# Optimization experiments

Hardware: AMD Instinct MI355X
Metric: run time of the kernel (lower is better)

The kernel has to match this reference:

```python
import jax, jax.numpy as jnp
import numpy as np

B = 8        # graphs per batch
N = 6000     # nodes per graph
DEG = 8      # avg degree -> E = B*N*DEG edges
K1, K2, K3 = 3600, 2160, 1080   # ceil(0.6*6000), ceil(0.6*3600), ceil(0.5*2160)
EPS = 1e-5
C_IN = 512


def gcn_conv(x, row, col, w, W, b):
    # GCNConv, normalize=True, add_self_loops=False. deg computed on col (target).
    n = x.shape[0]
    deg = jnp.zeros((n,), x.dtype).at[col].add(w)
    dinv = jnp.where(deg > 0, jax.lax.rsqrt(jnp.maximum(deg, 1e-12)), 0.0)
    norm = dinv[row] * w * dinv[col]                      # [E]
    h = x @ W                                             # [n, out]
    out = jnp.zeros_like(h).at[col].add(norm[:, None] * h[row])
    return out + b


def batch_norm(x, g, b):
    # track_running_stats=False -> always batch stats, biased variance
    mu = jnp.mean(x, 0)
    var = jnp.mean((x - mu) ** 2, 0)
    return (x - mu) * jax.lax.rsqrt(var + EPS) * g + b


def sag_pool(x, row, col, w, Wrel, Wroot, bias, n_per_graph, k):
    # SAGPooling: score = GraphConv(x, edge)->1, perm = per-graph top-k,
    # x = x[perm] * tanh(score[perm]); edges filtered (masked via weight 0 here).
    n = x.shape[0]
    agg = jnp.zeros_like(x).at[col].add(w[:, None] * x[row])
    score = (agg @ Wrel + x @ Wroot).squeeze(-1) + bias[0]        # [n]
    s2 = score.reshape(B, n_per_graph)
    _, topi = jax.lax.top_k(s2, k)                                # [B, k]
    perm = (topi + jnp.arange(B)[:, None] * n_per_graph).reshape(-1)
    x_new = x[perm] * jnp.tanh(score[perm])[:, None]
    inv = jnp.full((n,), -1, jnp.int32).at[perm].set(jnp.arange(B * k, dtype=jnp.int32))
    nrow = inv[row]
    ncol = inv[col]
    valid = (nrow >= 0) & (ncol >= 0) & (w > 0)
    w_new = jnp.where(valid, w, 0.0)
    nrow = jnp.where(valid, nrow, 0)
    ncol = jnp.where(valid, ncol, 0)
    return x_new, nrow, ncol, w_new


def setup_inputs() -> dict:
    key = jax.random.key(0)
    ks = jax.random.split(key, 32)
    x = jax.random.normal(ks[0], (B * N, C_IN), jnp.float32)
    src = jax.random.randint(ks[1], (B, N * DEG), 0, N)
    dst = jax.random.randint(ks[2], (B, N * DEG), 0, N)
    off = jnp.arange(B)[:, None] * N
    edge_index = jnp.stack([(src + off).reshape(-1), (dst + off).reshape(-1)]).astype(jnp.int32)

    def lin(k, cin, cout):
        return jax.random.normal(k, (cin, cout), jnp.float32) * (1.0 / np.sqrt(cin))

    inp = {
        'x': x, 'edge_index': edge_index,
        'W1': lin(ks[3], 512, 512), 'b1': jnp.zeros((512,), jnp.float32),
        'g1': jnp.ones((512,), jnp.float32), 'be1': jnp.zeros((512,), jnp.float32),
        'p1_rel': lin(ks[4], 512, 1), 'p1_root': lin(ks[5], 512, 1), 'p1_b': jnp.zeros((1,), jnp.float32),
        'W2': lin(ks[6], 512, 512), 'b2': jnp.zeros((512,), jnp.float32),
        'g2': jnp.ones((512,), jnp.float32), 'be2': jnp.zeros((512,), jnp.float32),
        'p2_rel': lin(ks[7], 512, 1), 'p2_root': lin(ks[8], 512, 1), 'p2_b': jnp.zeros((1,), jnp.float32),
        'W3': lin(ks[9], 512, 256), 'b3': jnp.zeros((256,), jnp.float32),
        'g3': jnp.ones((256,), jnp.float32), 'be3': jnp.zeros((256,), jnp.float32),
        'p3_rel': lin(ks[10], 256, 1), 'p3_root': lin(ks[11], 256, 1), 'p3_b': jnp.zeros((1,), jnp.float32),
        'W4': lin(ks[12], 256, 256), 'b4': jnp.zeros((256,), jnp.float32),
        'fcW': lin(ks[13], 512, 1), 'fcb': jnp.zeros((1,), jnp.float32),
    }
    return inp


def reference(x, edge_index, W1, b1, g1, be1, p1_rel, p1_root, p1_b,
              W2, b2, g2, be2, p2_rel, p2_root, p2_b,
              W3, b3, g3, be3, p3_rel, p3_root, p3_b,
              W4, b4, fcW, fcb):
    row, col = edge_index[0], edge_index[1]
    w = jnp.ones((row.shape[0],), jnp.float32)

    h = jax.nn.relu(batch_norm(gcn_conv(x, row, col, w, W1, b1), g1, be1))
    h, row, col, w = sag_pool(h, row, col, w, p1_rel, p1_root, p1_b, N, K1)

    h = jax.nn.relu(batch_norm(gcn_conv(h, row, col, w, W2, b2), g2, be2))
    h, row, col, w = sag_pool(h, row, col, w, p2_rel, p2_root, p2_b, K1, K2)

    h = jax.nn.relu(batch_norm(gcn_conv(h, row, col, w, W3, b3), g3, be3))
    h, row, col, w = sag_pool(h, row, col, w, p3_rel, p3_root, p3_b, K2, K3)

    h = gcn_conv(h, row, col, w, W4, b4)        # [B*K3, 256]
    g = h.reshape(B, K3, 256)
    feature = jnp.concatenate([g.max(axis=1), g.mean(axis=1)], axis=1)  # [B, 512]
    out = feature @ fcW + fcb
    return out, feature
```

## Files before the change

kernel.cpp:

```cpp
#include <hip/hip_runtime.h>
#include <cstdint>
#include <cstddef>

#define NB 8
#define NPG0 6000
#define N0 48000
#define NE 384000
#define KP1 3600
#define KP2 2160
#define KP3 1080

typedef __attribute__((ext_vector_type(8))) short short8;
typedef __attribute__((ext_vector_type(4))) float f32x4;
typedef __attribute__((ext_vector_type(4))) unsigned int u32x4;

__device__ inline ushort f2bf(float v) {
  unsigned u = __float_as_uint(v);
  u += 0x7FFF + ((u >> 16) & 1);
  return (ushort)(u >> 16);
}
__device__ inline float bf2f(ushort h) { return __uint_as_float(((unsigned)h) << 16); }

__global__ void split_kernel(const float* __restrict__ x, ushort* __restrict__ hi,
                             ushort* __restrict__ lo, size_t n4) {
  size_t i = (size_t)blockIdx.x * blockDim.x + threadIdx.x;
  size_t stride = (size_t)gridDim.x * blockDim.x;
  for (; i < n4; i += stride) {
    float4 v = ((const float4*)x)[i];
    ushort4 h, l;
    h.x = f2bf(v.x); l.x = f2bf(v.x - bf2f(h.x));
    h.y = f2bf(v.y); l.y = f2bf(v.y - bf2f(h.y));
    h.z = f2bf(v.z); l.z = f2bf(v.z - bf2f(h.z));
    h.w = f2bf(v.w); l.w = f2bf(v.w - bf2f(h.w));
    ((ushort4*)hi)[i] = h;
    ((ushort4*)lo)[i] = l;
  }
}

__global__ void wsplit_kernel(const float* __restrict__ W, ushort* __restrict__ hiT,
                              ushort* __restrict__ loT, int K, int N) {
  __shared__ float tile[32][33];
  int k0 = blockIdx.y * 32, n0 = blockIdx.x * 32;
  int tx = threadIdx.x;
  for (int dy = threadIdx.y; dy < 32; dy += 8)
    tile[dy][tx] = W[(size_t)(k0 + dy) * N + n0 + tx];
  __syncthreads();
  for (int dy = threadIdx.y; dy < 32; dy += 8) {
    float v = tile[tx][dy];
    ushort h = f2bf(v);
    ushort l = f2bf(v - bf2f(h));
    hiT[(size_t)(n0 + dy) * K + k0 + tx] = h;
    loT[(size_t)(n0 + dy) * K + k0 + tx] = l;
  }
}

__global__ __launch_bounds__(256) void gemm_split(
    const ushort* __restrict__ Ahi, const ushort* __restrict__ Alo,
    const ushort* __restrict__ BThi, const ushort* __restrict__ BTlo,
    float* __restrict__ C, int M, int K, int N, int mblocks) {
  __shared__ u32x4 lds4[2048];
  const int tid = threadIdx.x;
  const int mblk = blockIdx.x % mblocks;
  const int nblk = blockIdx.x / mblocks;
  const int bm = mblk * 128, bn = nblk * 128;
  const int lane = tid & 63;
  const int w = tid >> 6;
  const int wr = w >> 1, wc = w & 1;

  const ushort* sptr[8];
  int ldschunk[8];
#pragma unroll
  for (int i = 0; i < 8; ++i) {
    int idx = i * 256 + tid;
    int g = idx >> 9;
    int p = idx & 511;
    int r = p >> 2, pc = p & 3;
    int grow;
    const ushort* base;
    if (g == 0)      { base = Ahi;  grow = min(bm + r, M - 1); }
    else if (g == 1) { base = Alo;  grow = min(bm + r, M - 1); }
    else if (g == 2) { base = BThi; grow = bn + r; }
    else             { base = BTlo; grow = bn + r; }
    sptr[i] = base + (size_t)grow * K + pc * 8;
    int swz = (r & 3) ^ ((r >> 2) & 3);
    ldschunk[i] = g * 512 + r * 4 + (pc ^ swz);
  }

  f32x4 acc[4][4];
#pragma unroll
  for (int m = 0; m < 4; ++m)
#pragma unroll
    for (int n = 0; n < 4; ++n) acc[m][n] = (f32x4){0.f, 0.f, 0.f, 0.f};

  u32x4 st[8];
#pragma unroll
  for (int i = 0; i < 8; ++i) st[i] = *(const u32x4*)(sptr[i]);

  const int nk = K >> 5;
  for (int t = 0; t < nk; ++t) {
    __syncthreads();
#pragma unroll
    for (int i = 0; i < 8; ++i) lds4[ldschunk[i]] = st[i];
    if (t + 1 < nk) {
#pragma unroll
      for (int i = 0; i < 8; ++i) st[i] = *(const u32x4*)(sptr[i] + (size_t)(t + 1) * 32);
    }
    __syncthreads();

    const int kb = lane >> 4;
    const int l15 = lane & 15;
    short8 bh[4], bl[4];
#pragma unroll
    for (int n = 0; n < 4; ++n) {
      int rB = wc * 64 + n * 16 + l15;
      int swz = (rB & 3) ^ ((rB >> 2) & 3);
      int ch = rB * 4 + (kb ^ swz);
      bh[n] = *(const short8*)&lds4[1024 + ch];
      bl[n] = *(const short8*)&lds4[1536 + ch];
    }
#pragma unroll
    for (int m = 0; m < 4; ++m) {
      int rA = wr * 64 + m * 16 + l15;
      int swz = (rA & 3) ^ ((rA >> 2) & 3);
      int ch = rA * 4 + (kb ^ swz);
      short8 ah = *(const short8*)&lds4[ch];
      short8 al = *(const short8*)&lds4[512 + ch];
#pragma unroll
      for (int n = 0; n < 4; ++n) {
        acc[m][n] = __builtin_amdgcn_mfma_f32_16x16x32_bf16(ah, bh[n], acc[m][n], 0, 0, 0);
        acc[m][n] = __builtin_amdgcn_mfma_f32_16x16x32_bf16(ah, bl[n], acc[m][n], 0, 0, 0);
        acc[m][n] = __builtin_amdgcn_mfma_f32_16x16x32_bf16(al, bh[n], acc[m][n], 0, 0, 0);
      }
    }
  }

#pragma unroll
  for (int m = 0; m < 4; ++m) {
    int gr0 = bm + wr * 64 + m * 16 + ((lane >> 4) << 2);
#pragma unroll
    for (int j = 0; j < 4; ++j) {
      int gr = gr0 + j;
      if (gr < M) {
#pragma unroll
        for (int n = 0; n < 4; ++n) {
          C[(size_t)gr * N + bn + wc * 64 + n * 16 + (lane & 15)] = acc[m][n][j];
        }
      }
    }
  }
}

__global__ void edge_count_kernel(const int* __restrict__ col, const float* __restrict__ w,
                                  int E, int* __restrict__ counts) {
  int i = blockIdx.x * blockDim.x + threadIdx.x;
  if (i >= E) return;
  if (w && !(w[i] > 0.f)) return;
  atomicAdd(&counts[col[i]], 1);
}

__global__ __launch_bounds__(1024) void scan_kernel(const int* __restrict__ counts,
                                                    int* __restrict__ offsets, int n) {
  __shared__ int wsum[16];
  int tid = threadIdx.x;
  int per = (n + 1023) / 1024;
  int beg = tid * per;
  int end = min(beg + per, n);
  int s = 0;
  for (int i = beg; i < end; ++i) s += counts[i];
  int lane = tid & 63, wid = tid >> 6;
  int v = s;
  for (int off = 1; off < 64; off <<= 1) {
    int t = __shfl_up(v, off);
    if (lane >= off) v += t;
  }
  if (lane == 63) wsum[wid] = v;
  __syncthreads();
  if (wid == 0) {
    int wv = (lane < 16) ? wsum[lane] : 0;
    for (int off = 1; off < 16; off <<= 1) {
      int t = __shfl_up(wv, off);
      if (lane >= off) wv += t;
    }
    if (lane < 16) wsum[lane] = wv;
  }
  __syncthreads();
  int base = (v - s) + (wid > 0 ? wsum[wid - 1] : 0);
  int run = base;
  for (int i = beg; i < end; ++i) {
    offsets[i] = run;
    run += counts[i];
  }
  if (tid == 1023) offsets[n] = run;
}

__global__ void csr_fill_kernel(const int* __restrict__ row, const int* __restrict__ col,
                                const float* __restrict__ w, int E,
                                const int* __restrict__ offsets, int* __restrict__ fill,
                                int* __restrict__ csr_src) {
  int i = blockIdx.x * blockDim.x + threadIdx.x;
  if (i >= E) return;
  if (w && !(w[i] > 0.f)) return;
  int c = col[i];
  int pos = offsets[c] + atomicAdd(&fill[c], 1);
  csr_src[pos] = row[i];
}

__global__ void dinv_kernel(const int* __restrict__ counts, float* __restrict__ dinv, int n) {
  int i = blockIdx.x * blockDim.x + threadIdx.x;
  if (i >= n) return;
  int c = counts[i];
  dinv[i] = (c > 0) ? (1.0f / sqrtf((float)c)) : 0.f;
}

__global__ __launch_bounds__(256) void gcn_gather_kernel(
    const float* __restrict__ G, const int* __restrict__ offsets,
    const int* __restrict__ csr_src, const float* __restrict__ dinv,
    const float* __restrict__ bias, float* __restrict__ out, int C, int n) {
  int wid = threadIdx.x >> 6, lane = threadIdx.x & 63;
  int t = blockIdx.x * 4 + wid;
  if (t >= n) return;
  int beg = offsets[t], end = offsets[t + 1];
  float dt = dinv[t];
  bool two = (C == 512);
  float4 acc0 = make_float4(0.f, 0.f, 0.f, 0.f);
  float4 acc1 = make_float4(0.f, 0.f, 0.f, 0.f);
  for (int e = beg; e < end; ++e) {
    int s = csr_src[e];
    float ds = dinv[s];
    const float4* hr = (const float4*)(G + (size_t)s * C);
    float4 v0 = hr[lane];
    acc0.x += ds * v0.x; acc0.y += ds * v0.y; acc0.z += ds * v0.z; acc0.w += ds * v0.w;
    if (two) {
      float4 v1 = hr[lane + 64];
      acc1.x += ds * v1.x; acc1.y += ds * v1.y; acc1.z += ds * v1.z; acc1.w += ds * v1.w;
    }
  }
  float4* op = (float4*)(out + (size_t)t * C);
  float4 b0 = bias ? ((const float4*)bias)[lane] : make_float4(0.f, 0.f, 0.f, 0.f);
  op[lane] = make_float4(dt * acc0.x + b0.x, dt * acc0.y + b0.y,
                         dt * acc0.z + b0.z, dt * acc0.w + b0.w);
  if (two) {
    op[lane + 64] = make_float4(dt * acc1.x, dt * acc1.y, dt * acc1.z, dt * acc1.w);
  }
}

__global__ __launch_bounds__(256) void bn_stats_kernel(
    const float* __restrict__ h, size_t n4, int C, float* __restrict__ sums) {
  __shared__ float ls[1024];
  for (int i = threadIdx.x; i < 2 * C; i += 256) ls[i] = 0.f;
  __syncthreads();
  const int c0 = (threadIdx.x * 4) & (C - 1);
  float s0 = 0.f, s1 = 0.f, s2 = 0.f, s3 = 0.f;
  float q0 = 0.f, q1 = 0.f, q2 = 0.f, q3 = 0.f;
  size_t i = (size_t)blockIdx.x * 256 + threadIdx.x;
  const size_t stride = (size_t)gridDim.x * 256;
  for (; i < n4; i += stride) {
    float4 v = ((const float4*)h)[i];
    s0 += v.x; q0 += v.x * v.x;
    s1 += v.y; q1 += v.y * v.y;
    s2 += v.z; q2 += v.z * v.z;
    s3 += v.w; q3 += v.w * v.w;
  }
  atomicAdd(&ls[c0 + 0], s0); atomicAdd(&ls[C + c0 + 0], q0);
  atomicAdd(&ls[c0 + 1], s1); atomicAdd(&ls[C + c0 + 1], q1);
  atomicAdd(&ls[c0 + 2], s2); atomicAdd(&ls[C + c0 + 2], q2);
  atomicAdd(&ls[c0 + 3], s3); atomicAdd(&ls[C + c0 + 3], q3);
  __syncthreads();
  for (int j = threadIdx.x; j < 2 * C; j += 256) atomicAdd(&sums[j], ls[j]);
}

__global__ void bn_finalize_kernel(const float* __restrict__ sums,
                                   const float* __restrict__ g,
                                   const float* __restrict__ be,
                                   int n, int C, float* __restrict__ ss) {
  int c = blockIdx.x * blockDim.x + threadIdx.x;
  if (c >= C) return;
  float inv_n = 1.0f / (float)n;
  float mean = sums[c] * inv_n;
  float var = sums[C + c] * inv_n - mean * mean;
  var = fmaxf(var, 0.f);
  float sc = g[c] * rsqrtf(var + 1e-5f);
  ss[c] = sc;
  ss[C + c] = be[c] - mean * sc;
}

__global__ __launch_bounds__(256) void bn_dots_kernel(
    float* __restrict__ h, const float* __restrict__ ss,
    const float* __restrict__ wrel, const float* __restrict__ wroot,
    float* __restrict__ u, float* __restrict__ rr, int n, int C) {
  int wid = threadIdx.x >> 6, lane = threadIdx.x & 63;
  int v = blockIdx.x * 4 + wid;
  if (v >= n) return;
  float4* hr = (float4*)(h + (size_t)v * C);
  int nf4 = C >> 2;
  float su = 0.f, sr = 0.f;
  for (int q = lane; q < nf4; q += 64) {
    float4 x = hr[q];
    int c = q << 2;
    float4 sc = *(const float4*)&ss[c];
    float4 sh = *(const float4*)&ss[C + c];
    x.x = fmaxf(fmaf(x.x, sc.x, sh.x), 0.f);
    x.y = fmaxf(fmaf(x.y, sc.y, sh.y), 0.f);
    x.z = fmaxf(fmaf(x.z, sc.z, sh.z), 0.f);
    x.w = fmaxf(fmaf(x.w, sc.w, sh.w), 0.f);
    hr[q] = x;
    float4 w1 = *(const float4*)&wrel[c];
    float4 w2 = *(const float4*)&wroot[c];
    su += x.x * w1.x + x.y * w1.y + x.z * w1.z + x.w * w1.w;
    sr += x.x * w2.x + x.y * w2.y + x.z * w2.z + x.w * w2.w;
  }
  for (int off = 32; off > 0; off >>= 1) {
    su += __shfl_down(su, off);
    sr += __shfl_down(sr, off);
  }
  if (lane == 0) {
    u[v] = su;
    rr[v] = sr;
  }
}

__global__ void score_kernel(const float* __restrict__ u, const float* __restrict__ rr,
                             const int* __restrict__ offsets, const int* __restrict__ csr_src,
                             const float* __restrict__ pb, float* __restrict__ score, int n) {
  int i = blockIdx.x * blockDim.x + threadIdx.x;
  if (i >= n) return;
  float s = rr[i] + pb[0];
  int beg = offsets[i], end = offsets[i + 1];
  for (int e = beg; e < end; ++e) s += u[csr_src[e]];
  score[i] = s;
}

__global__ __launch_bounds__(1024) void topk_radix_kernel(
    const float* __restrict__ score, int npg, int K, int* __restrict__ perm) {
  __shared__ unsigned sbuf[8192];
  __shared__ int tieL[6000];
  __shared__ int hist[256];
  __shared__ int wps[4];
  __shared__ unsigned sPref;
  __shared__ int sKrem, sAbove, sSel, sTie;
  int g = blockIdx.x;
  int tid = threadIdx.x;
  for (int i = tid; i < npg; i += 1024) {
    unsigned u = __float_as_uint(score[g * npg + i]);
    sbuf[i] = (u >> 31) ? ~u : (u | 0x80000000u);
  }
  if (tid == 0) { sPref = 0; sKrem = K; sAbove = 0; sSel = 0; sTie = 0; }
  __syncthreads();

  for (int pass = 0; pass < 4; ++pass) {
    int shift = 24 - 8 * pass;
    if (tid < 256) hist[tid] = 0;
    unsigned prefLoc = sPref;
    int kRemLoc = sKrem;
    __syncthreads();
    for (int i = tid; i < npg; i += 1024) {
      unsigned k = sbuf[i];
      if (pass == 0 || (k >> (shift + 8)) == prefLoc)
        atomicAdd(&hist[(k >> shift) & 255], 1);
    }
    __syncthreads();
    int v = 0, a = 0;
    if (tid < 256) {
      a = hist[255 - tid];
      v = a;
      int lane = tid & 63;
      for (int off = 1; off < 64; off <<= 1) {
        int t2 = __shfl_up(v, off);
        if (lane >= off) v += t2;
      }
      if (lane == 63) wps[tid >> 6] = v;
    }
    __syncthreads();
    if (tid < 256) {
      int w4 = tid >> 6;
      int incl = v;
      for (int q = 0; q < w4; ++q) incl += wps[q];
      int gt = incl - a;
      if (gt < kRemLoc && kRemLoc <= incl) {
        int d = 255 - tid;
        sPref = (prefLoc << 8) | (unsigned)d;
        sAbove += gt;
        sKrem = kRemLoc - gt;
      }
    }
    __syncthreads();
  }

  unsigned T = sPref;
  int above = sAbove;
  for (int i = tid; i < npg; i += 1024) {
    unsigned k = sbuf[i];
    if (k > T) {
      int p = atomicAdd(&sSel, 1);
      perm[g * K + p] = g * npg + i;
    } else if (k == T) {
      int p = atomicAdd(&sTie, 1);
      tieL[p] = i;
    }
  }
  __syncthreads();
  int r = sKrem, tc = sTie;
  if (r == tc) {
    for (int j = tid; j < r; j += 1024) perm[g * K + above + j] = g * npg + tieL[j];
  } else {
    int p2 = 1;
    while (p2 < tc) p2 <<= 1;
    for (int i = tid; i < p2; i += 1024) sbuf[i] = (i < tc) ? (unsigned)tieL[i] : 0xFFFFFFFFu;
    __syncthreads();
    for (int k2 = 2; k2 <= p2; k2 <<= 1) {
      for (int j = k2 >> 1; j > 0; j >>= 1) {
        for (int i = tid; i < p2; i += 1024) {
          int l = i ^ j;
          if (l > i) {
            unsigned a2 = sbuf[i], b2 = sbuf[l];
            bool up = ((i & k2) == 0);
            if (up ? (a2 > b2) : (a2 < b2)) { sbuf[i] = b2; sbuf[l] = a2; }
          }
        }
        __syncthreads();
      }
    }
    for (int j = tid; j < r; j += 1024) perm[g * K + above + j] = g * npg + (int)sbuf[j];
  }
}

__global__ void inv_set_kernel(const int* __restrict__ perm, int* __restrict__ inv, int m) {
  int i = blockIdx.x * blockDim.x + threadIdx.x;
  if (i < m) inv[perm[i]] = i;
}

__global__ void xnew_split_kernel(const float* __restrict__ h, const float* __restrict__ score,
                                  const int* __restrict__ perm, ushort* __restrict__ xhi,
                                  ushort* __restrict__ xlo, int C) {
  int i = blockIdx.x;
  int old = perm[i];
  float tv = tanhf(score[old]);
  const float4* src = (const float4*)(h + (size_t)old * C);
  int c4 = C >> 2;
  for (int c = threadIdx.x; c < c4; c += blockDim.x) {
    float4 v = src[c];
    v.x *= tv; v.y *= tv; v.z *= tv; v.w *= tv;
    ushort4 hh, ll;
    hh.x = f2bf(v.x); ll.x = f2bf(v.x - bf2f(hh.x));
    hh.y = f2bf(v.y); ll.y = f2bf(v.y - bf2f(hh.y));
    hh.z = f2bf(v.z); ll.z = f2bf(v.z - bf2f(hh.z));
    hh.w = f2bf(v.w); ll.w = f2bf(v.w - bf2f(hh.w));
    ((ushort4*)(xhi + (size_t)i * C))[c] = hh;
    ((ushort4*)(xlo + (size_t)i * C))[c] = ll;
  }
}

__global__ void edge_remap_count_kernel(const int* __restrict__ row, const int* __restrict__ col,
                                        const float* __restrict__ w, const int* __restrict__ inv,
                                        int E, int* __restrict__ nrow, int* __restrict__ ncol,
                                        float* __restrict__ nw, int* __restrict__ counts) {
  int i = blockIdx.x * blockDim.x + threadIdx.x;
  if (i >= E) return;
  float wv = w ? w[i] : 1.f;
  int nr = inv[row[i]];
  int nc = inv[col[i]];
  bool valid = (nr >= 0) && (nc >= 0) && (wv > 0.f);
  nrow[i] = valid ? nr : 0;
  ncol[i] = valid ? nc : 0;
  nw[i] = valid ? wv : 0.f;
  if (valid) atomicAdd(&counts[nc], 1);
}

__global__ void final_pool_kernel(const float* __restrict__ h, float* __restrict__ dout) {
  int g = blockIdx.x;
  int c = threadIdx.x;
  const float* base = h + ((size_t)g * KP3) * 256 + c;
  float mx = -3.402823466e38f, sm = 0.f;
  for (int r = 0; r < KP3; ++r) {
    float v = base[(size_t)r * 256];
    mx = fmaxf(mx, v);
    sm += v;
  }
  dout[8 + g * 512 + c] = mx;
  dout[8 + g * 512 + 256 + c] = sm * (1.0f / (float)KP3);
}

__global__ void fc_kernel(const float* __restrict__ feat, const float* __restrict__ fcW,
                          const float* __restrict__ fcb, float* __restrict__ dout) {
  int g = blockIdx.x;
  int lane = threadIdx.x;
  float s = 0.f;
  for (int c = lane; c < 512; c += 64) s += feat[g * 512 + c] * fcW[c];
  for (int off = 32; off > 0; off >>= 1) s += __shfl_down(s, off);
  if (lane == 0) dout[g] = s + fcb[0];
}

static inline size_t alignup(size_t x) { return (x + 255) & ~(size_t)255; }

extern "C" void kernel_launch(void* const* d_in, const int* in_sizes, int n_in,
                              void* d_out, int out_size, void* d_ws, size_t ws_size,
                              hipStream_t stream) {
  (void)in_sizes; (void)n_in; (void)out_size; (void)ws_size;
  const float* x0 = (const float*)d_in[0];
  const int* ei = (const int*)d_in[1];
  const int* row0 = ei;
  const int* col0 = ei + NE;
  const float* W1 = (const float*)d_in[2];
  const float* g1 = (const float*)d_in[4];
  const float* be1 = (const float*)d_in[5];
  const float* p1rel = (const float*)d_in[6];
  const float* p1root = (const float*)d_in[7];
  const float* p1b = (const float*)d_in[8];
  const float* W2 = (const float*)d_in[9];
  const float* g2 = (const float*)d_in[11];
  const float* be2 = (const float*)d_in[12];
  const float* p2rel = (const float*)d_in[13];
  const float* p2root = (const float*)d_in[14];
  const float* p2b = (const float*)d_in[15];
  const float* W3 = (const float*)d_in[16];
  const float* g3 = (const float*)d_in[18];
  const float* be3 = (const float*)d_in[19];
  const float* p3rel = (const float*)d_in[20];
  const float* p3root = (const float*)d_in[21];
  const float* p3b = (const float*)d_in[22];
  const float* W4 = (const float*)d_in[23];
  const float* b4 = (const float*)d_in[24];
  const float* fcW = (const float*)d_in[25];
  const float* fcb = (const float*)d_in[26];
  float* out = (float*)d_out;

  char* ws = (char*)d_ws;
  size_t off = 0;
  auto alloc = [&](size_t bytes) {
    char* p = ws + off;
    off = alignup(off + bytes);
    return p;
  };
  float* RegA = (float*)alloc((size_t)N0 * 512 * 4);
  float* RegB = (float*)alloc((size_t)N0 * 512 * 4);
  ushort* Ahi = (ushort*)alloc((size_t)N0 * 512 * 2);
  ushort* Alo = (ushort*)alloc((size_t)N0 * 512 * 2);
  int* rowA = (int*)alloc((size_t)NE * 4);
  int* colA = (int*)alloc((size_t)NE * 4);
  float* wA = (float*)alloc((size_t)NE * 4);
  int* rowB = (int*)alloc((size_t)NE * 4);
  int* colB = (int*)alloc((size_t)NE * 4);
  float* wB = (float*)alloc((size_t)NE * 4);
  int* csr_src = (int*)alloc((size_t)NE * 4);
  int* offsets = (int*)alloc((size_t)(N0 + 1) * 4);
  int* counts = (int*)alloc((size_t)N0 * 4);
  int* fill = (int*)alloc((size_t)N0 * 4);
  float* dinv = (float*)alloc((size_t)N0 * 4);
  float* scoreb = (float*)alloc((size_t)N0 * 4);
  float* ubuf = (float*)alloc((size_t)N0 * 4);
  float* rbuf = (float*)alloc((size_t)N0 * 4);
  int* perm = (int*)alloc((size_t)NB * KP1 * 4);
  int* inv = (int*)alloc((size_t)N0 * 4);
  float* bnsums = (float*)alloc(1024 * 4);
  float* bnss = (float*)alloc(1024 * 4);
  ushort* wt1h = (ushort*)alloc(512 * 512 * 2);
  ushort* wt1l = (ushort*)alloc(512 * 512 * 2);
  ushort* wt2h = (ushort*)alloc(512 * 512 * 2);
  ushort* wt2l = (ushort*)alloc(512 * 512 * 2);
  ushort* wt3h = (ushort*)alloc(256 * 512 * 2);
  ushort* wt3l = (ushort*)alloc(256 * 512 * 2);
  ushort* wt4h = (ushort*)alloc(256 * 256 * 2);
  ushort* wt4l = (ushort*)alloc(256 * 256 * 2);

  const int n1 = NB * KP1;
  const int n2 = NB * KP2;
  const int n3 = NB * KP3;

  auto build_csr_rest = [&](const int* row, const int* col, const float* w, int n) {
    hipMemsetAsync(fill, 0, (size_t)n * 4, stream);
    scan_kernel<<<1, 1024, 0, stream>>>(counts, offsets, n);
    csr_fill_kernel<<<(NE + 255) / 256, 256, 0, stream>>>(row, col, w, NE, offsets, fill, csr_src);
    dinv_kernel<<<(n + 255) / 256, 256, 0, stream>>>(counts, dinv, n);
  };

  auto bn_relu_dots = [&](float* h, int n, int C, const float* g, const float* be,
                          const float* wrel, const float* wroot) {
    hipMemsetAsync(bnsums, 0, 4096, stream);
    size_t n4 = (size_t)n * C / 4;
    int nblk = (int)min((n4 + 255) / 256, (size_t)512);
    bn_stats_kernel<<<nblk, 256, 0, stream>>>(h, n4, C, bnsums);
    bn_finalize_kernel<<<(C + 255) / 256, 256, 0, stream>>>(bnsums, g, be, n, C, bnss);
    bn_dots_kernel<<<(n + 3) / 4, 256, 0, stream>>>(h, bnss, wrel, wroot, ubuf, rbuf, n, C);
  };

  auto gemm = [&](const ushort* ah, const ushort* al, const ushort* bth, const ushort* btl,
                  float* Cout, int M, int K, int N) {
    int mblocks = (M + 127) / 128;
    int nblocks = N / 128;
    gemm_split<<<mblocks * nblocks, 256, 0, stream>>>(ah, al, bth, btl, Cout, M, K, N, mblocks);
  };

  auto pool = [&](const float* h, int n, int C, int npg, int K, const float* pb, int nNext,
                  const int* erow, const int* ecol, const float* ew,
                  int* nrow, int* ncol, float* nw) {
    score_kernel<<<(n + 255) / 256, 256, 0, stream>>>(ubuf, rbuf, offsets, csr_src, pb, scoreb, n);
    topk_radix_kernel<<<NB, 1024, 0, stream>>>(scoreb, npg, K, perm);
    hipMemsetAsync(inv, 0xFF, (size_t)n * 4, stream);
    hipMemsetAsync(counts, 0, (size_t)nNext * 4, stream);
    inv_set_kernel<<<(NB * K + 255) / 256, 256, 0, stream>>>(perm, inv, NB * K);
    xnew_split_kernel<<<NB * K, 128, 0, stream>>>(h, scoreb, perm, Ahi, Alo, C);
    edge_remap_count_kernel<<<(NE + 255) / 256, 256, 0, stream>>>(erow, ecol, ew, inv, NE,
                                                                  nrow, ncol, nw, counts);
  };

  wsplit_kernel<<<dim3(512 / 32, 512 / 32), dim3(32, 8), 0, stream>>>(W1, wt1h, wt1l, 512, 512);
  wsplit_kernel<<<dim3(512 / 32, 512 / 32), dim3(32, 8), 0, stream>>>(W2, wt2h, wt2l, 512, 512);
  wsplit_kernel<<<dim3(256 / 32, 512 / 32), dim3(32, 8), 0, stream>>>(W3, wt3h, wt3l, 512, 256);
  wsplit_kernel<<<dim3(256 / 32, 256 / 32), dim3(32, 8), 0, stream>>>(W4, wt4h, wt4l, 256, 256);
  split_kernel<<<4096, 256, 0, stream>>>(x0, Ahi, Alo, (size_t)N0 * 512 / 4);

  hipMemsetAsync(counts, 0, (size_t)N0 * 4, stream);
  edge_count_kernel<<<(NE + 255) / 256, 256, 0, stream>>>(col0, nullptr, NE, counts);
  build_csr_rest(row0, col0, nullptr, N0);
  gemm(Ahi, Alo, wt1h, wt1l, RegA, N0, 512, 512);
  gcn_gather_kernel<<<(N0 + 3) / 4, 256, 0, stream>>>(RegA, offsets, csr_src, dinv, nullptr,
                                                      RegB, 512, N0);
  bn_relu_dots(RegB, N0, 512, g1, be1, p1rel, p1root);
  pool(RegB, N0, 512, NPG0, KP1, p1b, n1, row0, col0, nullptr, rowA, colA, wA);

  build_csr_rest(rowA, colA, wA, n1);
  gemm(Ahi, Alo, wt2h, wt2l, RegA, n1, 512, 512);
  gcn_gather_kernel<<<(n1 + 3) / 4, 256, 0, stream>>>(RegA, offsets, csr_src, dinv, nullptr,
                                                      RegB, 512, n1);
  bn_relu_dots(RegB, n1, 512, g2, be2, p2rel, p2root);
  pool(RegB, n1, 512, KP1, KP2, p2b, n2, rowA, colA, wA, rowB, colB, wB);

  build_csr_rest(rowB, colB, wB, n2);
  gemm(Ahi, Alo, wt3h, wt3l, RegA, n2, 512, 256);
  gcn_gather_kernel<<<(n2 + 3) / 4, 256, 0, stream>>>(RegA, offsets, csr_src, dinv, nullptr,
                                                      RegB, 256, n2);
  bn_relu_dots(RegB, n2, 256, g3, be3, p3rel, p3root);
  pool(RegB, n2, 256, KP2, KP3, p3b, n3, rowB, colB, wB, rowA, colA, wA);

  build_csr_rest(rowA, colA, wA, n3);
  gemm(Ahi, Alo, wt4h, wt4l, RegA, n3, 256, 256);
  gcn_gather_kernel<<<(n3 + 3) / 4, 256, 0, stream>>>(RegA, offsets, csr_src, dinv, b4,
                                                      RegB, 256, n3);

  final_pool_kernel<<<NB, 256, 0, stream>>>(RegB, out);
  fc_kernel<<<NB, 64, 0, stream>>>(out + 8, fcW, fcb, out);
}
```

Baseline: 1.064 ms.

## Use direct global-to-LDS double buffering in GEMM and fuse small graph kernels

The split-bf16 GEMM now loads tiles with global_load_lds straight into a double-buffered LDS region, prefetching the next K slice during compute and dropping one barrier per iteration. The dinv computation moves into the scan kernel and the inv scatter into xnew_split, which removes two launches per stage. The gather kernel interleaves blocks across graphs and unrolls its edge loop by two for more memory-level parallelism. The costs are doubled LDS per block, which may lower occupancy, and the gather grid now assumes node counts divisible by four.

```diff
diff --git a/kernel.cpp b/kernel.cpp
--- a/kernel.cpp
+++ b/kernel.cpp
@@ -20,6 +20,12 @@
   return (ushort)(u >> 16);
 }
 __device__ inline float bf2f(ushort h) { return __uint_as_float(((unsigned)h) << 16); }
+
+__device__ __forceinline__ void glds16(const void* g, void* l) {
+  __builtin_amdgcn_global_load_lds(
+      (const __attribute__((address_space(1))) unsigned int*)g,
+      (__attribute__((address_space(3))) unsigned int*)l, 16, 0, 0);
+}
 
 __global__ void split_kernel(const float* __restrict__ x, ushort* __restrict__ hi,
                              ushort* __restrict__ lo, size_t n4) {
@@ -58,32 +64,26 @@
     const ushort* __restrict__ Ahi, const ushort* __restrict__ Alo,
     const ushort* __restrict__ BThi, const ushort* __restrict__ BTlo,
     float* __restrict__ C, int M, int K, int N, int mblocks) {
-  __shared__ u32x4 lds4[2048];
+  __shared__ u32x4 lds4[4096];
   const int tid = threadIdx.x;
+  const int lane = tid & 63;
+  const int w = tid >> 6;
   const int mblk = blockIdx.x % mblocks;
   const int nblk = blockIdx.x / mblocks;
   const int bm = mblk * 128, bn = nblk * 128;
-  const int lane = tid & 63;
-  const int w = tid >> 6;
   const int wr = w >> 1, wc = w & 1;
 
-  const ushort* sptr[8];
-  int ldschunk[8];
-#pragma unroll
-  for (int i = 0; i < 8; ++i) {
-    int idx = i * 256 + tid;
-    int g = idx >> 9;
-    int p = idx & 511;
-    int r = p >> 2, pc = p & 3;
-    int grow;
-    const ushort* base;
-    if (g == 0)      { base = Ahi;  grow = min(bm + r, M - 1); }
-    else if (g == 1) { base = Alo;  grow = min(bm + r, M - 1); }
-    else if (g == 2) { base = BThi; grow = bn + r; }
-    else             { base = BTlo; grow = bn + r; }
-    sptr[i] = base + (size_t)grow * K + pc * 8;
-    int swz = (r & 3) ^ ((r >> 2) & 3);
-    ldschunk[i] = g * 512 + r * 4 + (pc ^ swz);
+  const ushort* srcp[8];
+  {
+    const ushort* base = (w == 0) ? Ahi : (w == 1) ? Alo : (w == 2) ? BThi : BTlo;
+    #pragma unroll
+    for (int i = 0; i < 8; ++i) {
+      int r = i * 16 + (lane >> 2);
+      int swz = (r & 3) ^ ((r >> 2) & 3);
+      int pcs = (lane & 3) ^ swz;
+      int grow = (w < 2) ? min(bm + r, M - 1) : (bn + r);
+      srcp[i] = base + (size_t)grow * K + pcs * 8;
+    }
   }
 
   f32x4 acc[4][4];
@@ -92,39 +92,39 @@
 #pragma unroll
     for (int n = 0; n < 4; ++n) acc[m][n] = (f32x4){0.f, 0.f, 0.f, 0.f};
 
-  u32x4 st[8];
-#pragma unroll
-  for (int i = 0; i < 8; ++i) st[i] = *(const u32x4*)(sptr[i]);
-
   const int nk = K >> 5;
+  const int kb = lane >> 4;
+  const int l15 = lane & 15;
+
+#pragma unroll
+  for (int i = 0; i < 8; ++i) glds16(srcp[i], &lds4[w * 512 + i * 64]);
+  __syncthreads();
+
+  int cur = 0;
   for (int t = 0; t < nk; ++t) {
-    __syncthreads();
-#pragma unroll
-    for (int i = 0; i < 8; ++i) lds4[ldschunk[i]] = st[i];
     if (t + 1 < nk) {
-#pragma unroll
-      for (int i = 0; i < 8; ++i) st[i] = *(const u32x4*)(sptr[i] + (size_t)(t + 1) * 32);
-    }
-    __syncthreads();
-
-    const int kb = lane >> 4;
-    const int l15 = lane & 15;
+      int nb = (cur ^ 1) * 2048;
+#pragma unroll
+      for (int i = 0; i < 8; ++i)
+        glds16(srcp[i] + (size_t)(t + 1) * 32, &lds4[nb + w * 512 + i * 64]);
+    }
+    const int bb = cur * 2048;
     short8 bh[4], bl[4];
 #pragma unroll
     for (int n = 0; n < 4; ++n) {
       int rB = wc * 64 + n * 16 + l15;
       int swz = (rB & 3) ^ ((rB >> 2) & 3);
       int ch = rB * 4 + (kb ^ swz);
-      bh[n] = *(const short8*)&lds4[1024 + ch];
-      bl[n] = *(const short8*)&lds4[1536 + ch];
+      bh[n] = *(const short8*)&lds4[bb + 1024 + ch];
+      bl[n] = *(const short8*)&lds4[bb + 1536 + ch];
     }
 #pragma unroll
     for (int m = 0; m < 4; ++m) {
       int rA = wr * 64 + m * 16 + l15;
       int swz = (rA & 3) ^ ((rA >> 2) & 3);
       int ch = rA * 4 + (kb ^ swz);
-      short8 ah = *(const short8*)&lds4[ch];
-      short8 al = *(const short8*)&lds4[512 + ch];
+      short8 ah = *(const short8*)&lds4[bb + ch];
+      short8 al = *(const short8*)&lds4[bb + 512 + ch];
 #pragma unroll
       for (int n = 0; n < 4; ++n) {
         acc[m][n] = __builtin_amdgcn_mfma_f32_16x16x32_bf16(ah, bh[n], acc[m][n], 0, 0, 0);
@@ -132,6 +132,8 @@
         acc[m][n] = __builtin_amdgcn_mfma_f32_16x16x32_bf16(al, bh[n], acc[m][n], 0, 0, 0);
       }
     }
+    __syncthreads();
+    cur ^= 1;
   }
 
 #pragma unroll
@@ -159,7 +161,8 @@
 }
 
 __global__ __launch_bounds__(1024) void scan_kernel(const int* __restrict__ counts,
-                                                    int* __restrict__ offsets, int n) {
+                                                    int* __restrict__ offsets,
+                                                    float* __restrict__ dinv, int n) {
   __shared__ int wsum[16];
   int tid = threadIdx.x;
   int per = (n + 1023) / 1024;
@@ -188,7 +191,9 @@
   int run = base;
   for (int i = beg; i < end; ++i) {
     offsets[i] = run;
-    run += counts[i];
+    int c = counts[i];
+    run += c;
+    dinv[i] = (c > 0) ? rsqrtf((float)c) : 0.f;
   }
   if (tid == 1023) offsets[n] = run;
 }
@@ -205,34 +210,46 @@
   csr_src[pos] = row[i];
 }
 
-__global__ void dinv_kernel(const int* __restrict__ counts, float* __restrict__ dinv, int n) {
-  int i = blockIdx.x * blockDim.x + threadIdx.x;
-  if (i >= n) return;
-  int c = counts[i];
-  dinv[i] = (c > 0) ? (1.0f / sqrtf((float)c)) : 0.f;
-}
-
 __global__ __launch_bounds__(256) void gcn_gather_kernel(
     const float* __restrict__ G, const int* __restrict__ offsets,
     const int* __restrict__ csr_src, const float* __restrict__ dinv,
-    const float* __restrict__ bias, float* __restrict__ out, int C, int n) {
+    const float* __restrict__ bias, float* __restrict__ out, int C, int n, int npg) {
   int wid = threadIdx.x >> 6, lane = threadIdx.x & 63;
-  int t = blockIdx.x * 4 + wid;
+  int g = blockIdx.x & 7;
+  int local = blockIdx.x >> 3;
+  int t = g * npg + local * 4 + wid;
   if (t >= n) return;
   int beg = offsets[t], end = offsets[t + 1];
   float dt = dinv[t];
   bool two = (C == 512);
   float4 acc0 = make_float4(0.f, 0.f, 0.f, 0.f);
   float4 acc1 = make_float4(0.f, 0.f, 0.f, 0.f);
-  for (int e = beg; e < end; ++e) {
-    int s = csr_src[e];
-    float ds = dinv[s];
-    const float4* hr = (const float4*)(G + (size_t)s * C);
-    float4 v0 = hr[lane];
-    acc0.x += ds * v0.x; acc0.y += ds * v0.y; acc0.z += ds * v0.z; acc0.w += ds * v0.w;
+  int e = beg;
+  for (; e + 2 <= end; e += 2) {
+    int s0 = csr_src[e], s1 = csr_src[e + 1];
+    float d0 = dinv[s0], d1 = dinv[s1];
+    const float4* h0 = (const float4*)(G + (size_t)s0 * C);
+    const float4* h1 = (const float4*)(G + (size_t)s1 * C);
+    float4 a0 = h0[lane];
+    float4 b0 = h1[lane];
+    acc0.x += d0 * a0.x; acc0.y += d0 * a0.y; acc0.z += d0 * a0.z; acc0.w += d0 * a0.w;
+    acc0.x += d1 * b0.x; acc0.y += d1 * b0.y; acc0.z += d1 * b0.z; acc0.w += d1 * b0.w;
     if (two) {
-      float4 v1 = hr[lane + 64];
-      acc1.x += ds * v1.x; acc1.y += ds * v1.y; acc1.z += ds * v1.z; acc1.w += ds * v1.w;
+      float4 a1 = h0[lane + 64];
+      float4 b1 = h1[lane + 64];
+      acc1.x += d0 * a1.x; acc1.y += d0 * a1.y; acc1.z += d0 * a1.z; acc1.w += d0 * a1.w;
+      acc1.x += d1 * b1.x; acc1.y += d1 * b1.y; acc1.z += d1 * b1.z; acc1.w += d1 * b1.w;
+    }
+  }
+  if (e < end) {
+    int s0 = csr_src[e];
+    float d0 = dinv[s0];
+    const float4* h0 = (const float4*)(G + (size_t)s0 * C);
+    float4 a0 = h0[lane];
+    acc0.x += d0 * a0.x; acc0.y += d0 * a0.y; acc0.z += d0 * a0.z; acc0.w += d0 * a0.w;
+    if (two) {
+      float4 a1 = h0[lane + 64];
+      acc1.x += d0 * a1.x; acc1.y += d0 * a1.y; acc1.z += d0 * a1.z; acc1.w += d0 * a1.w;
     }
   }
   float4* op = (float4*)(out + (size_t)t * C);
@@ -424,16 +441,12 @@
   }
 }
 
-__global__ void inv_set_kernel(const int* __restrict__ perm, int* __restrict__ inv, int m) {
-  int i = blockIdx.x * blockDim.x + threadIdx.x;
-  if (i < m) inv[perm[i]] = i;
-}
-
 __global__ void xnew_split_kernel(const float* __restrict__ h, const float* __restrict__ score,
                                   const int* __restrict__ perm, ushort* __restrict__ xhi,
-                                  ushort* __restrict__ xlo, int C) {
+                                  ushort* __restrict__ xlo, int* __restrict__ inv, int C) {
   int i = blockIdx.x;
   int old = perm[i];
+  if (threadIdx.x == 0) inv[old] = i;
   float tv = tanhf(score[old]);
   const float4* src = (const float4*)(h + (size_t)old * C);
   int c4 = C >> 2;
@@ -568,9 +581,8 @@
 
   auto build_csr_rest = [&](const int* row, const int* col, const float* w, int n) {
     hipMemsetAsync(fill, 0, (size_t)n * 4, stream);
-    scan_kernel<<<1, 1024, 0, stream>>>(counts, offsets, n);
+    scan_kernel<<<1, 1024, 0, stream>>>(counts, offsets, dinv, n);
     csr_fill_kernel<<<(NE + 255) / 256, 256, 0, stream>>>(row, col, w, NE, offsets, fill, csr_src);
-    dinv_kernel<<<(n + 255) / 256, 256, 0, stream>>>(counts, dinv, n);
   };
 
   auto bn_relu_dots = [&](float* h, int n, int C, const float* g, const float* be,
@@ -597,8 +609,7 @@
     topk_radix_kernel<<<NB, 1024, 0, stream>>>(scoreb, npg, K, perm);
     hipMemsetAsync(inv, 0xFF, (size_t)n * 4, stream);
     hipMemsetAsync(counts, 0, (size_t)nNext * 4, stream);
-    inv_set_kernel<<<(NB * K + 255) / 256, 256, 0, stream>>>(perm, inv, NB * K);
-    xnew_split_kernel<<<NB * K, 128, 0, stream>>>(h, scoreb, perm, Ahi, Alo, C);
+    xnew_split_kernel<<<NB * K, 128, 0, stream>>>(h, scoreb, perm, Ahi, Alo, inv, C);
     edge_remap_count_kernel<<<(NE + 255) / 256, 256, 0, stream>>>(erow, ecol, ew, inv, NE,
                                                                   nrow, ncol, nw, counts);
   };
@@ -613,29 +624,29 @@
   edge_count_kernel<<<(NE + 255) / 256, 256, 0, stream>>>(col0, nullptr, NE, counts);
   build_csr_rest(row0, col0, nullptr, N0);
   gemm(Ahi, Alo, wt1h, wt1l, RegA, N0, 512, 512);
-  gcn_gather_kernel<<<(N0 + 3) / 4, 256, 0, stream>>>(RegA, offsets, csr_src, dinv, nullptr,
-                                                      RegB, 512, N0);
+  gcn_gather_kernel<<<N0 / 4, 256, 0, stream>>>(RegA, offsets, csr_src, dinv, nullptr,
+                                                RegB, 512, N0, NPG0);
   bn_relu_dots(RegB, N0, 512, g1, be1, p1rel, p1root);
   pool(RegB, N0, 512, NPG0, KP1, p1b, n1, row0, col0, nullptr, rowA, colA, wA);
 
   build_csr_rest(rowA, colA, wA, n1);
   gemm(Ahi, Alo, wt2h, wt2l, RegA, n1, 512, 512);
-  gcn_gather_kernel<<<(n1 + 3) / 4, 256, 0, stream>>>(RegA, offsets, csr_src, dinv, nullptr,
-                                                      RegB, 512, n1);
+  gcn_gather_kernel<<<n1 / 4, 256, 0, stream>>>(RegA, offsets, csr_src, dinv, nullptr,
+                                                RegB, 512, n1, KP1);
   bn_relu_dots(RegB, n1, 512, g2, be2, p2rel, p2root);
   pool(RegB, n1, 512, KP1, KP2, p2b, n2, rowA, colA, wA, rowB, colB, wB);
 
   build_csr_rest(rowB, colB, wB, n2);
   gemm(Ahi, Alo, wt3h, wt3l, RegA, n2, 512, 256);
-  gcn_gather_kernel<<<(n2 + 3) / 4, 256, 0, stream>>>(RegA, offsets, csr_src, dinv, nullptr,
-                                                      RegB, 256, n2);
+  gcn_gather_kernel<<<n2 / 4, 256, 0, stream>>>(RegA, offsets, csr_src, dinv, nullptr,
+                                                RegB, 256, n2, KP2);
   bn_relu_dots(RegB, n2, 256, g3, be3, p3rel, p3root);
   pool(RegB, n2, 256, KP2, KP3, p3b, n3, rowB, colB, wB, rowA, colA, wA);
 
   build_csr_rest(rowA, colA, wA, n3);
   gemm(Ahi, Alo, wt4h, wt4l, RegA, n3, 256, 256);
-  gcn_gather_kernel<<<(n3 + 3) / 4, 256, 0, stream>>>(RegA, offsets, csr_src, dinv, b4,
-                                                      RegB, 256, n3);
+  gcn_gather_kernel<<<n3 / 4, 256, 0, stream>>>(RegA, offsets, csr_src, dinv, b4,
+                                                RegB, 256, n3, KP3);
 
   final_pool_kernel<<<NB, 256, 0, stream>>>(RegB, out);
   fc_kernel<<<NB, 64, 0, stream>>>(out + 8, fcW, fcb, out);
```

Result: no change. 1.073 ms (+0.9%).
